# Kernel optimization log

Hardware: AMD Instinct MI355X
Metric: run time of the kernel (lower is better)

## Reference

```python
import jax, jax.numpy as jnp
import numpy as np

BS, N, D_ENT, K, D_IN, D_F, H, L, S = 128, 512, 256, 128, 1024, 256, 128, 2, 64
MAX_ENTITY_NUM = 512.0
TEMP = 1.0
NEG = -1e9


def _ln(x, g, b, eps=1e-5):
    m = jnp.mean(x, -1, keepdims=True)
    v = jnp.mean((x - m) ** 2, -1, keepdims=True)
    return (x - m) * jax.lax.rsqrt(v + eps) * g + b


def setup_inputs() -> dict:
    key = jax.random.key(0)
    ks = jax.random.split(key, 16)
    nrm = lambda k, sh, s=0.02: jax.random.normal(k, sh, jnp.float32) * s
    entity_num = jax.random.randint(ks[0], (BS,), 64, N)
    selected_units = jax.random.randint(ks[1], (BS, S), 0, N + 1) % (entity_num[:, None] + 1)
    selected_units_num = jax.random.randint(ks[2], (BS,), 1, S + 1).at[0].set(S)  # max == S so torch seq_len == S
    return dict(
        embedding=nrm(ks[3], (BS, D_IN), 1.0),
        entity_embedding=nrm(ks[4], (BS, N, D_ENT), 1.0),
        key_w=nrm(ks[5], (K, D_ENT)), key_b=jnp.zeros((K,), jnp.float32),
        q1_w=nrm(ks[6], (D_F, D_IN)), q1_b=jnp.zeros((D_F,), jnp.float32),
        q2_w=nrm(ks[7], (K, D_F)), q2_b=jnp.zeros((K,), jnp.float32),
        e1_w=nrm(ks[8], (D_F, K)), e1_b=jnp.zeros((D_F,), jnp.float32),
        e2_w=nrm(ks[9], (D_IN, D_F)), e2_b=jnp.zeros((D_IN,), jnp.float32),
        end_embedding=nrm(ks[10], (1, K), 0.09),
        lstm_wih=nrm(ks[11], (L, 4 * H, K)),
        lstm_whh=nrm(ks[12], (L, 4 * H, H)),
        ln_ig=jnp.ones((L, 4 * H), jnp.float32), ln_ib=jnp.zeros((L, 4 * H), jnp.float32),
        ln_hg=jnp.ones((L, 4 * H), jnp.float32), ln_hb=jnp.zeros((L, 4 * H), jnp.float32),
        ln_cg=jnp.ones((L, H), jnp.float32), ln_cb=jnp.zeros((L, H), jnp.float32),
        entity_num=entity_num, selected_units=selected_units, selected_units_num=selected_units_num,
    )


def _forward(embedding, entity_embedding, key_w, key_b, q1_w, q1_b, q2_w, q2_b,
             e1_w, e1_b, e2_w, e2_b, end_embedding, lstm_wih, lstm_whh,
             ln_ig, ln_ib, ln_hg, ln_hb, ln_cg, ln_cb,
             entity_num, selected_units, selected_units_num):
    bs = embedding.shape[0]
    ar = jnp.arange(bs)
    # keys: [bs, N+1, K] with end-embedding placed at position entity_num
    key = jnp.einsum('bnd,kd->bnk', entity_embedding, key_w) + key_b
    key = jnp.concatenate([key, jnp.zeros((bs, 1, K), key.dtype)], axis=1)
    key = key.at[ar, entity_num].set(end_embedding[0])
    # entity_reduce_type == 'constant': key_embeddings = embed_mlp(key / MAX_ENTITY_NUM)
    kr = key / MAX_ENTITY_NUM
    key_emb = jax.nn.relu(jnp.einsum('bnk,fk->bnf', kr, e1_w) + e1_b)
    key_emb = jnp.einsum('bnf,df->bnd', key_emb, e2_w) + e2_b  # [bs, N+1, D_IN]
    # precompute per-step masks (cumulative disabling of previously selected units;
    # end token blocked only at step 0, then re-enabled unless selected)
    init_mask = jnp.arange(N + 1)[None, :] < (entity_num + 1)[:, None]
    oh = jax.nn.one_hot(selected_units, N + 1, dtype=jnp.int32)
    prev = jnp.cumsum(oh, axis=1) - oh  # selected strictly before step i
    mask_seq = init_mask[:, None, :] & (prev == 0)  # [bs, S, N+1]
    mask_seq = mask_seq.at[ar, 0, entity_num].set(False)

    def step(carry, xs):
        ae, hs, cs = carry
        i, su_i, m_i = xs
        # query MLP
        x = jax.nn.relu(ae @ q1_w.T + q1_b) @ q2_w.T + q2_b  # [bs, K]
        new_hs, new_cs = [], []
        for l in range(L):  # layer-norm LSTM stack
            gates = _ln(x @ lstm_wih[l].T, ln_ig[l], ln_ib[l]) + _ln(hs[l] @ lstm_whh[l].T, ln_hg[l], ln_hb[l])
            ig, fg, gg, og = jnp.split(gates, 4, axis=-1)
            c = _ln(jax.nn.sigmoid(fg) * cs[l] + jax.nn.sigmoid(ig) * jnp.tanh(gg), ln_cg[l], ln_cb[l])
            h = jax.nn.sigmoid(og) * jnp.tanh(c)
            new_hs.append(h); new_cs.append(c)
            x = h
        logits = jnp.where(m_i, jnp.einsum('bk,bnk->bn', x, key) / TEMP, NEG)
        gate = ((i + 1) <= selected_units_num) & (su_i != entity_num)
        ae = ae + key_emb[ar, su_i] * gate[:, None].astype(ae.dtype)
        return (ae, jnp.stack(new_hs), jnp.stack(new_cs)), logits

    hs0 = jnp.zeros((L, bs, H), embedding.dtype)
    cs0 = jnp.zeros((L, bs, H), embedding.dtype)
    (ae, _, _), logits = jax.lax.scan(
        step, (embedding, hs0, cs0),
        (jnp.arange(S), selected_units.T, jnp.swapaxes(mask_seq, 0, 1)))
    return jnp.swapaxes(logits, 0, 1), ae  # logits [bs, S, N+1]


def reference(embedding, entity_embedding, key_w, key_b, q1_w, q1_b, q2_w, q2_b,
              e1_w, e1_b, e2_w, e2_b, end_embedding, lstm_wih, lstm_whh,
              ln_ig, ln_ib, ln_hg, ln_hb, ln_cg, ln_cb,
              entity_num, selected_units, selected_units_num):
    logits, ae = _forward(embedding, entity_embedding, key_w, key_b, q1_w, q1_b, q2_w, q2_b,
                          e1_w, e1_b, e2_w, e2_b, end_embedding, lstm_wih, lstm_whh,
                          ln_ig, ln_ib, ln_hg, ln_hb, ln_cg, ln_cb,
                          entity_num, selected_units, selected_units_num)
    # torch forward returns (logits, units=None, embedding, selected_units_num); units omitted here
    return logits, ae, selected_units_num
```

## Files before the change

kernel.cpp:

```cpp
#include <hip/hip_runtime.h>
#include <hip/hip_bf16.h>
#include <math.h>

#define BSZ   128
#define NENT  512
#define NP1   513
#define DENT  256
#define KDIM  128
#define DIN   1024
#define DF    256
#define HDIM  128
#define SSTEP 64
#define G4    512
#define NEGV  (-1e9f)
#define INV_MAX (1.0f/512.0f)

typedef float v2f __attribute__((ext_vector_type(2)));
typedef __attribute__((ext_vector_type(8))) short bf16x8;
typedef __attribute__((ext_vector_type(4))) float f32x4;

__device__ inline float sigf(float x){ return 1.f/(1.f+__expf(-x)); }
__device__ inline float tanh_fast(float x){ float e=__expf(2.f*x); return 1.f - 2.f/(e+1.f); }

__device__ inline float wave_sum_partial(float x){
  x += __int_as_float(__builtin_amdgcn_update_dpp(0, __float_as_int(x), 0x111, 0xf, 0xf, true));
  x += __int_as_float(__builtin_amdgcn_update_dpp(0, __float_as_int(x), 0x112, 0xf, 0xf, true));
  x += __int_as_float(__builtin_amdgcn_update_dpp(0, __float_as_int(x), 0x114, 0xf, 0xf, true));
  x += __int_as_float(__builtin_amdgcn_update_dpp(0, __float_as_int(x), 0x118, 0xf, 0xf, true));
  x += __int_as_float(__builtin_amdgcn_update_dpp(0, __float_as_int(x), 0x142, 0xa, 0xf, true));
  x += __int_as_float(__builtin_amdgcn_update_dpp(0, __float_as_int(x), 0x143, 0xc, 0xf, true));
  return x;
}
__device__ inline float wave_sum(float x){
  return __int_as_float(__builtin_amdgcn_readlane(__float_as_int(wave_sum_partial(x)), 63));
}

__device__ inline unsigned pk8(float4 f){
  int r = 0;
  r = __builtin_amdgcn_cvt_pk_fp8_f32(f.x, f.y, r, false);
  r = __builtin_amdgcn_cvt_pk_fp8_f32(f.z, f.w, r, true);
  return (unsigned)r;
}
__device__ inline float dot4_fp8(unsigned w, float4 h, float acc){
  v2f p = __builtin_amdgcn_cvt_pk_f32_fp8((int)w, false);
  acc = fmaf(p.x, h.x, acc); acc = fmaf(p.y, h.y, acc);
  p = __builtin_amdgcn_cvt_pk_f32_fp8((int)w, true);
  acc = fmaf(p.x, h.z, acc); acc = fmaf(p.y, h.w, acc);
  return acc;
}

__device__ inline float2 block_reduce2(float x, float y, float* red){
  float sx0 = wave_sum_partial(x), sy0 = wave_sum_partial(y);
  int w = threadIdx.x>>6;
  __syncthreads();
  if((threadIdx.x&63)==63){ red[w]=sx0; red[8+w]=sy0; }
  __syncthreads();
  float sx=0.f, sy=0.f;
  #pragma unroll
  for(int q=0;q<8;q++){ sx+=red[q]; sy+=red[8+q]; }
  return make_float2(sx,sy);
}

template<bool BKMAJOR, bool RELU, bool GATHER>
__global__ __launch_bounds__(256)
void mfma_gemm(const float* __restrict__ A, const float* __restrict__ B,
               const float* __restrict__ bias, float* __restrict__ C,
               int M, int N, int K,
               const int* __restrict__ gidx, float scale){
  __shared__ ushort Abf[64][72];
  __shared__ ushort Bbf[64][72];
  const int t = threadIdx.x;
  const int bm = blockIdx.x, bn = blockIdx.y;
  const int w = t>>6, l = t&63;
  const int lm = l&15, lg = l>>4;
  const int r0 = w*16;
  f32x4 acc[4];
  #pragma unroll
  for(int f=0;f<4;f++) acc[f] = (f32x4){0.f,0.f,0.f,0.f};

  for(int k0=0;k0<K;k0+=64){
    #pragma unroll
    for(int i=0;i<4;i++){
      int idx = t + i*256;
      int row = idx>>4, c4 = (idx&15)<<2;
      const float* src;
      if(GATHER){
        int gr = bm*64+row;
        src = &A[((size_t)(gr>>6)*NP1 + gidx[gr])*(size_t)K + k0 + c4];
      } else {
        src = &A[((size_t)bm*64+row)*K + k0 + c4];
      }
      float4 v = *(const float4*)src;
      if(GATHER){ v.x*=scale; v.y*=scale; v.z*=scale; v.w*=scale; }
      ushort4 u;
      u.x = __float_as_uint(v.x)>>16; u.y = __float_as_uint(v.y)>>16;
      u.z = __float_as_uint(v.z)>>16; u.w = __float_as_uint(v.w)>>16;
      *(ushort4*)&Abf[row][c4] = u;
    }
    if(!BKMAJOR){
      #pragma unroll
      for(int i=0;i<4;i++){
        int idx = t + i*256;
        int row = idx>>4, c4 = (idx&15)<<2;
        float4 v = *(const float4*)&B[((size_t)bn*64+row)*K + k0 + c4];
        ushort4 u;
        u.x = __float_as_uint(v.x)>>16; u.y = __float_as_uint(v.y)>>16;
        u.z = __float_as_uint(v.z)>>16; u.w = __float_as_uint(v.w)>>16;
        *(ushort4*)&Bbf[row][c4] = u;
      }
    } else {
      #pragma unroll
      for(int i=0;i<4;i++){
        int idx = t + i*256;
        int kr = idx>>4, n4 = (idx&15)<<2;
        float4 v = *(const float4*)&B[(size_t)(k0+kr)*N + bn*64 + n4];
        Bbf[n4+0][kr] = __float_as_uint(v.x)>>16;
        Bbf[n4+1][kr] = __float_as_uint(v.y)>>16;
        Bbf[n4+2][kr] = __float_as_uint(v.z)>>16;
        Bbf[n4+3][kr] = __float_as_uint(v.w)>>16;
      }
    }
    __syncthreads();
    #pragma unroll
    for(int kk=0;kk<64;kk+=32){
      bf16x8 a = *(const bf16x8*)&Abf[r0+lm][kk + lg*8];
      #pragma unroll
      for(int f=0;f<4;f++){
        bf16x8 b = *(const bf16x8*)&Bbf[f*16+lm][kk + lg*8];
        acc[f] = __builtin_amdgcn_mfma_f32_16x16x32_bf16(a, b, acc[f], 0,0,0);
      }
    }
    __syncthreads();
  }
  #pragma unroll
  for(int f=0;f<4;f++){
    int gcol = bn*64 + f*16 + lm;
    float bb = bias ? bias[gcol] : 0.f;
    #pragma unroll
    for(int r=0;r<4;r++){
      int grow = bm*64 + r0 + lg*4 + r;
      float v = acc[f][r] + bb;
      if(RELU) v = fmaxf(v, 0.f);
      C[(size_t)grow*N + gcol] = v;
    }
  }
}

__global__ __launch_bounds__(256)
void key_gemm_mfma(const float* __restrict__ A, const float* __restrict__ W,
                   const float* __restrict__ bias, float* __restrict__ C){
  __shared__ ushort Abf[64][264];
  __shared__ ushort Bbf[128][264];
  __shared__ float bs[128];
  const int t = threadIdx.x;
  const int bm = blockIdx.x;
  #pragma unroll
  for(int i=0;i<16;i++){
    int idx = t + i*256;
    int row = idx>>6, c4 = (idx&63)<<2;
    float4 v = *(const float4*)&A[((size_t)bm*64+row)*256 + c4];
    ushort4 u;
    u.x = __float_as_uint(v.x)>>16; u.y = __float_as_uint(v.y)>>16;
    u.z = __float_as_uint(v.z)>>16; u.w = __float_as_uint(v.w)>>16;
    *(ushort4*)&Abf[row][c4] = u;
  }
  #pragma unroll
  for(int i=0;i<32;i++){
    int idx = t + i*256;
    int row = idx>>6, c4 = (idx&63)<<2;
    float4 v = *(const float4*)&W[(size_t)row*256 + c4];
    ushort4 u;
    u.x = __float_as_uint(v.x)>>16; u.y = __float_as_uint(v.y)>>16;
    u.z = __float_as_uint(v.z)>>16; u.w = __float_as_uint(v.w)>>16;
    *(ushort4*)&Bbf[row][c4] = u;
  }
  if(t<128) bs[t] = bias[t];
  __syncthreads();
  const int w = t>>6, l = t&63;
  const int lm = l&15, lg = l>>4;
  const int r0 = w*16;
  f32x4 acc[8];
  #pragma unroll
  for(int f=0;f<8;f++) acc[f] = (f32x4){0.f,0.f,0.f,0.f};
  #pragma unroll
  for(int k0=0;k0<256;k0+=32){
    bf16x8 a = *(const bf16x8*)&Abf[r0+lm][k0 + lg*8];
    #pragma unroll
    for(int f=0;f<8;f++){
      bf16x8 b = *(const bf16x8*)&Bbf[f*16+lm][k0 + lg*8];
      acc[f] = __builtin_amdgcn_mfma_f32_16x16x32_bf16(a, b, acc[f], 0,0,0);
    }
  }
  #pragma unroll
  for(int f=0;f<8;f++){
    int gcol = f*16 + lm;
    float bb = bs[gcol];
    #pragma unroll
    for(int r=0;r<4;r++){
      int grow = bm*64 + r0 + lg*4 + r;
      size_t orow = (size_t)(grow>>9)*NP1 + (grow&511);
      C[orow*KDIM + gcol] = acc[f][r] + bb;
    }
  }
}

__global__ void fixup_end(const int* __restrict__ en, const float* __restrict__ end_emb,
                          float* __restrict__ key){
  int b = blockIdx.x, k = threadIdx.x;
  int e = en[b];
  key[((size_t)b*NP1 + NENT)*KDIM + k] = 0.f;
  key[((size_t)b*NP1 + e)*KDIM + k] = end_emb[k];
}

__global__ __launch_bounds__(256)
void c0_kernel(const float* __restrict__ q1_w, const float* __restrict__ e2_b,
               float* __restrict__ c0v){
  __shared__ float red[4];
  int f = blockIdx.x, t = threadIdx.x;
  float4 a = *(const float4*)&q1_w[(size_t)f*DIN + t*4];
  float4 e = *(const float4*)&e2_b[t*4];
  float p = a.x*e.x + a.y*e.y + a.z*e.z + a.w*e.w;
  float s = wave_sum_partial(p);
  if((t&63)==63) red[t>>6] = s;
  __syncthreads();
  if(t==0) c0v[f] = red[0]+red[1]+red[2]+red[3];
}

__global__ void prefix_kernel(const float* __restrict__ U0, const float* __restrict__ Q1K,
                              const float* __restrict__ c0v, const float* __restrict__ T1,
                              const int* __restrict__ su, const int* __restrict__ en,
                              const int* __restrict__ sun,
                              float* __restrict__ RU, float* __restrict__ s1,
                              float* __restrict__ ngout){
  int b = blockIdx.x, f = threadIdx.x;
  float acc = U0[b*DF+f];
  float c0f = c0v[f];
  float s1a = 0.f, ng = 0.f;
  int enb = en[b], sunb = sun[b];
  for(int j=0;j<SSTEP;j++){
    int r = b*SSTEP+j;
    float q = Q1K[(size_t)r*DF+f];
    float tt = T1[(size_t)r*DF+f];
    RU[(size_t)r*DF+f] = fmaxf(acc,0.f);
    int sj = su[r];
    float g = ((j+1)<=sunb && sj!=enb) ? 1.f : 0.f;
    acc = fmaf(g, q + c0f, acc);
    s1a = fmaf(g, tt, s1a);
    ng += g;
  }
  s1[b*DF+f]=s1a;
  if(f==0) ngout[b]=ng;
}

__global__ __launch_bounds__(512)
void ln512(float* __restrict__ G, const float* __restrict__ gam, const float* __restrict__ bet){
  __shared__ float red[16];
  size_t r = blockIdx.x;
  int j = threadIdx.x;
  float v = G[r*G4+j];
  float2 s = block_reduce2(v, v*v, red);
  float mu = s.x*(1.f/512.f);
  float rs = rsqrtf(s.y*(1.f/512.f) - mu*mu + 1e-5f);
  G[r*G4+j] = (v-mu)*rs*gam[j] + bet[j];
}

__global__ __launch_bounds__(512)
__attribute__((amdgpu_waves_per_eu(2,2)))
void lstm_serial(const float* __restrict__ wih, const float* __restrict__ whh,
                 const float* __restrict__ G0,
                 const float* __restrict__ ln_ig, const float* __restrict__ ln_ib,
                 const float* __restrict__ ln_hg, const float* __restrict__ ln_hb,
                 const float* __restrict__ ln_cg, const float* __restrict__ ln_cb,
                 float* __restrict__ H1){
  const int b = blockIdx.x;
  const int j = threadIdx.x;
  __shared__ uint4 W0s8[8][512];
  __shared__ uint4 W1s8[8][512];
  __shared__ float h0s[128], h1s[128];
  __shared__ float pvv[512], pv1[512];
  __shared__ float lnA[512], lnB[512], lnC[512], lnD[512], lnE[512], lnF[512];
  __shared__ float red[32];

  #pragma unroll
  for(int c=0;c<8;c++){
    const float* s0 = &whh[(size_t)j*KDIM + c*16];
    uint4 p;
    p.x = pk8(*(const float4*)(s0+ 0));
    p.y = pk8(*(const float4*)(s0+ 4));
    p.z = pk8(*(const float4*)(s0+ 8));
    p.w = pk8(*(const float4*)(s0+12));
    W0s8[c][j] = p;
    const float* s1 = &wih[65536 + (size_t)j*KDIM + c*16];
    uint4 q;
    q.x = pk8(*(const float4*)(s1+ 0));
    q.y = pk8(*(const float4*)(s1+ 4));
    q.z = pk8(*(const float4*)(s1+ 8));
    q.w = pk8(*(const float4*)(s1+12));
    W1s8[c][j] = q;
  }
  uint4 w2p[8];
  #pragma unroll
  for(int c=0;c<8;c++){
    const float* s2 = &whh[65536 + (size_t)j*KDIM + c*16];
    w2p[c].x = pk8(*(const float4*)(s2+ 0));
    w2p[c].y = pk8(*(const float4*)(s2+ 4));
    w2p[c].z = pk8(*(const float4*)(s2+ 8));
    w2p[c].w = pk8(*(const float4*)(s2+12));
  }
  lnA[j] = ln_hg[j];     lnB[j] = ln_hb[j];
  lnC[j] = ln_ig[512+j]; lnD[j] = ln_ib[512+j];
  lnE[j] = ln_hg[512+j]; lnF[j] = ln_hb[512+j];

  float cg0A=0.f,cb0A=0.f,cg0B=0.f,cb0B=0.f;
  float cg1A=0.f,cb1A=0.f,cg1B=0.f,cb1B=0.f;
  float c0rA=0.f,c0rB=0.f,c1rA=0.f,c1rB=0.f;
  if(j<64){
    cg0A=ln_cg[j];      cb0A=ln_cb[j];
    cg0B=ln_cg[j+64];   cb0B=ln_cb[j+64];
    cg1A=ln_cg[128+j];    cb1A=ln_cb[128+j];
    cg1B=ln_cg[128+j+64]; cb1B=ln_cb[128+j+64];
  }
  if(j<128){ h0s[j]=0.f; h1s[j]=0.f; }
  __syncthreads();

  const float4* h04 = (const float4*)h0s;
  const float4* h14 = (const float4*)h1s;
  const int w = j>>6;

  for(int i=0;i<SSTEP;i++){
    float g0a[4], g0b[4];
    if(j<64){
      const float* gp = &G0[((size_t)b*SSTEP+i)*G4];
      #pragma unroll
      for(int k=0;k<4;k++){ g0a[k]=gp[j+128*k]; g0b[k]=gp[j+64+128*k]; }
    }

    float v = 0.f, vb = 0.f;
    #pragma unroll
    for(int c=0;c<8;c++){
      uint4 ww = W0s8[c][j];
      v  = dot4_fp8(ww.x, h04[4*c+0], v );
      vb = dot4_fp8(ww.y, h04[4*c+1], vb);
      v  = dot4_fp8(ww.z, h04[4*c+2], v );
      vb = dot4_fp8(ww.w, h04[4*c+3], vb);
    }
    v += vb;
    float v1 = 0.f, v1b = 0.f;
    #pragma unroll
    for(int c=0;c<8;c++){
      uint4 ww = w2p[c];
      v1  = dot4_fp8(ww.x, h14[4*c+0], v1 );
      v1b = dot4_fp8(ww.y, h14[4*c+1], v1b);
      v1  = dot4_fp8(ww.z, h14[4*c+2], v1 );
      v1b = dot4_fp8(ww.w, h14[4*c+3], v1b);
    }
    v1 += v1b;
    {
      float a  = wave_sum_partial(v);
      float bq = wave_sum_partial(v*v);
      float c2 = wave_sum_partial(v1);
      float d  = wave_sum_partial(v1*v1);
      if((j&63)==63){ red[w]=a; red[8+w]=bq; red[16+w]=c2; red[24+w]=d; }
    }
    pvv[j]=v; pv1[j]=v1;
    __syncthreads();

    if(j<64){
      float S=0.f,S2=0.f;
      #pragma unroll
      for(int q=0;q<8;q++){ S+=red[q]; S2+=red[8+q]; }
      float mu = S*(1.f/512.f);
      float rs = rsqrtf(S2*(1.f/512.f) - mu*mu + 1e-5f);
      float ashA[4], ashB[4];
      #pragma unroll
      for(int k=0;k<4;k++){
        int ia = j + 128*k, ib = j + 64 + 128*k;
        ashA[k] = g0a[k] + (pvv[ia]-mu)*rs*lnA[ia] + lnB[ia];
        ashB[k] = g0b[k] + (pvv[ib]-mu)*rs*lnA[ib] + lnB[ib];
      }
      float cpA = sigf(ashA[1])*c0rA + sigf(ashA[0])*tanh_fast(ashA[2]);
      float cpB = sigf(ashB[1])*c0rB + sigf(ashB[0])*tanh_fast(ashB[2]);
      float s  = wave_sum(cpA+cpB);
      float s2 = wave_sum(cpA*cpA+cpB*cpB);
      float muc = s*(1.f/128.f);
      float rsc = rsqrtf(s2*(1.f/128.f) - muc*muc + 1e-5f);
      c0rA = (cpA-muc)*rsc*cg0A + cb0A;
      c0rB = (cpB-muc)*rsc*cg0B + cb0B;
      h0s[j]    = sigf(ashA[3])*tanh_fast(c0rA);
      h0s[j+64] = sigf(ashB[3])*tanh_fast(c0rB);
    }
    __syncthreads();

    float u = 0.f, ub = 0.f;
    #pragma unroll
    for(int c=0;c<8;c++){
      uint4 ww = W1s8[c][j];
      u  = dot4_fp8(ww.x, h04[4*c+0], u );
      ub = dot4_fp8(ww.y, h04[4*c+1], ub);
      u  = dot4_fp8(ww.z, h04[4*c+2], u );
      ub = dot4_fp8(ww.w, h04[4*c+3], ub);
    }
    u += ub;
    {
      float a  = wave_sum_partial(u);
      float bq = wave_sum_partial(u*u);
      if((j&63)==63){ red[w]=a; red[8+w]=bq; }
    }
    pvv[j]=u;
    __syncthreads();

    if(j<64){
      float Su=0.f,Su2=0.f,Sv=0.f,Sv2=0.f;
      #pragma unroll
      for(int q=0;q<8;q++){ Su+=red[q]; Su2+=red[8+q]; Sv+=red[16+q]; Sv2+=red[24+q]; }
      float muu = Su*(1.f/512.f);
      float rsu = rsqrtf(Su2*(1.f/512.f) - muu*muu + 1e-5f);
      float muv = Sv*(1.f/512.f);
      float rsv = rsqrtf(Sv2*(1.f/512.f) - muv*muv + 1e-5f);
      float ashA[4], ashB[4];
      #pragma unroll
      for(int k=0;k<4;k++){
        int ia = j + 128*k, ib = j + 64 + 128*k;
        ashA[k] = (pvv[ia]-muu)*rsu*lnC[ia] + lnD[ia]
                + (pv1[ia]-muv)*rsv*lnE[ia] + lnF[ia];
        ashB[k] = (pvv[ib]-muu)*rsu*lnC[ib] + lnD[ib]
                + (pv1[ib]-muv)*rsv*lnE[ib] + lnF[ib];
      }
      float cpA = sigf(ashA[1])*c1rA + sigf(ashA[0])*tanh_fast(ashA[2]);
      float cpB = sigf(ashB[1])*c1rB + sigf(ashB[0])*tanh_fast(ashB[2]);
      float s  = wave_sum(cpA+cpB);
      float s2 = wave_sum(cpA*cpA+cpB*cpB);
      float muc = s*(1.f/128.f);
      float rsc = rsqrtf(s2*(1.f/128.f) - muc*muc + 1e-5f);
      c1rA = (cpA-muc)*rsc*cg1A + cb1A;
      c1rB = (cpB-muc)*rsc*cg1B + cb1B;
      float hA = sigf(ashA[3])*tanh_fast(c1rA);
      float hB = sigf(ashB[3])*tanh_fast(c1rB);
      h1s[j]    = hA;
      h1s[j+64] = hB;
      H1[((size_t)b*SSTEP+i)*HDIM + j]      = hA;
      H1[((size_t)b*SSTEP+i)*HDIM + j + 64] = hB;
    }
    __syncthreads();
  }
}

__global__ __launch_bounds__(512)
void logits_kernel(const float* __restrict__ key, const float* __restrict__ H1,
                   const int* __restrict__ en, const int* __restrict__ su,
                   float* __restrict__ out){
  const int b = blockIdx.x;
  const int ihalf = blockIdx.y;
  __shared__ float HsT[128][36];
  __shared__ int firstsel[NP1];
  for(int t=threadIdx.x; t<32*HDIM; t+=512){
    int il = t>>7, k = t&127;
    HsT[k][il] = H1[(size_t)b*SSTEP*HDIM + (size_t)(ihalf*32+il)*HDIM + k];
  }
  for(int t=threadIdx.x; t<NP1; t+=512) firstsel[t] = 1<<30;
  __syncthreads();
  if(threadIdx.x < SSTEP) atomicMin(&firstsel[su[b*SSTEP+threadIdx.x]], (int)threadIdx.x);
  __syncthreads();
  const int enb = en[b];
  const int tn = threadIdx.x & 255;
  const int ig = threadIdx.x >> 8;
  const int i0l = ig*16;
  const int ig0 = ihalf*32 + i0l;
  float acc0[16], acc1[16];
  #pragma unroll
  for(int q=0;q<16;q++){ acc0[q]=0.f; acc1[q]=0.f; }
  const float* kr0 = key + ((size_t)b*NP1 + tn)*KDIM;
  const float* kr1 = key + ((size_t)b*NP1 + tn + 256)*KDIM;
  for(int k=0;k<KDIM;k+=4){
    float4 kv0 = *(const float4*)&kr0[k];
    float4 kv1 = *(const float4*)&kr1[k];
    float k0a[4] = {kv0.x,kv0.y,kv0.z,kv0.w};
    float k1a[4] = {kv1.x,kv1.y,kv1.z,kv1.w};
    #pragma unroll
    for(int kk=0;kk<4;kk++){
      float4 h0 = *(const float4*)&HsT[k+kk][i0l+0];
      float4 h1 = *(const float4*)&HsT[k+kk][i0l+4];
      float4 h2 = *(const float4*)&HsT[k+kk][i0l+8];
      float4 h3 = *(const float4*)&HsT[k+kk][i0l+12];
      float ka = k0a[kk], kb = k1a[kk];
      acc0[ 0]=fmaf(ka,h0.x,acc0[ 0]); acc0[ 1]=fmaf(ka,h0.y,acc0[ 1]);
      acc0[ 2]=fmaf(ka,h0.z,acc0[ 2]); acc0[ 3]=fmaf(ka,h0.w,acc0[ 3]);
      acc0[ 4]=fmaf(ka,h1.x,acc0[ 4]); acc0[ 5]=fmaf(ka,h1.y,acc0[ 5]);
      acc0[ 6]=fmaf(ka,h1.z,acc0[ 6]); acc0[ 7]=fmaf(ka,h1.w,acc0[ 7]);
      acc0[ 8]=fmaf(ka,h2.x,acc0[ 8]); acc0[ 9]=fmaf(ka,h2.y,acc0[ 9]);
      acc0[10]=fmaf(ka,h2.z,acc0[10]); acc0[11]=fmaf(ka,h2.w,acc0[11]);
      acc0[12]=fmaf(ka,h3.x,acc0[12]); acc0[13]=fmaf(ka,h3.y,acc0[13]);
      acc0[14]=fmaf(ka,h3.z,acc0[14]); acc0[15]=fmaf(ka,h3.w,acc0[15]);
      acc1[ 0]=fmaf(kb,h0.x,acc1[ 0]); acc1[ 1]=fmaf(kb,h0.y,acc1[ 1]);
      acc1[ 2]=fmaf(kb,h0.z,acc1[ 2]); acc1[ 3]=fmaf(kb,h0.w,acc1[ 3]);
      acc1[ 4]=fmaf(kb,h1.x,acc1[ 4]); acc1[ 5]=fmaf(kb,h1.y,acc1[ 5]);
      acc1[ 6]=fmaf(kb,h1.z,acc1[ 6]); acc1[ 7]=fmaf(kb,h1.w,acc1[ 7]);
      acc1[ 8]=fmaf(kb,h2.x,acc1[ 8]); acc1[ 9]=fmaf(kb,h2.y,acc1[ 9]);
      acc1[10]=fmaf(kb,h2.z,acc1[10]); acc1[11]=fmaf(kb,h2.w,acc1[11]);
      acc1[12]=fmaf(kb,h3.x,acc1[12]); acc1[13]=fmaf(kb,h3.y,acc1[13]);
      acc1[14]=fmaf(kb,h3.z,acc1[14]); acc1[15]=fmaf(kb,h3.w,acc1[15]);
    }
  }
  const int n0 = tn, n1 = tn + 256;
  const int fs0 = firstsel[n0], fs1 = firstsel[n1];
  #pragma unroll
  for(int q=0;q<16;q++){
    int i = ig0 + q;
    bool m0 = (n0 <= enb) && (fs0 >= i) && !(i==0 && n0==enb);
    bool m1 = (n1 <= enb) && (fs1 >= i) && !(i==0 && n1==enb);
    out[((size_t)b*SSTEP + i)*NP1 + n0] = m0 ? acc0[q] : NEGV;
    out[((size_t)b*SSTEP + i)*NP1 + n1] = m1 ? acc1[q] : NEGV;
  }
  if(threadIdx.x < 32){
    int i = ihalf*32 + threadIdx.x;
    out[((size_t)b*SSTEP + i)*NP1 + 512] = NEGV;
  }
}

__global__ void ae_out_kernel(const float* __restrict__ emb, const float* __restrict__ P,
                              const float* __restrict__ e2_b, const float* __restrict__ ng,
                              const int* __restrict__ sun, float* __restrict__ out){
  const size_t AE_OFF = (size_t)BSZ*SSTEP*NP1;
  const size_t SUN_OFF = AE_OFF + (size_t)BSZ*DIN;
  int idx = blockIdx.x*256+threadIdx.x;
  int b = idx>>10, d = idx&1023;
  out[AE_OFF + idx] = emb[idx] + P[idx] + ng[b]*e2_b[d];
  if(idx < BSZ) out[SUN_OFF + idx] = (float)sun[idx];
}

extern "C" void kernel_launch(void* const* d_in, const int* in_sizes, int n_in,
                              void* d_out, int out_size, void* d_ws, size_t ws_size,
                              hipStream_t stream){
  const float* emb     = (const float*)d_in[0];
  const float* ent     = (const float*)d_in[1];
  const float* key_w   = (const float*)d_in[2];
  const float* key_b   = (const float*)d_in[3];
  const float* q1_w    = (const float*)d_in[4];
  const float* q1_b    = (const float*)d_in[5];
  const float* q2_w    = (const float*)d_in[6];
  const float* q2_b    = (const float*)d_in[7];
  const float* e1_w    = (const float*)d_in[8];
  const float* e1_b    = (const float*)d_in[9];
  const float* e2_w    = (const float*)d_in[10];
  const float* e2_b    = (const float*)d_in[11];
  const float* end_emb = (const float*)d_in[12];
  const float* wih     = (const float*)d_in[13];
  const float* whh     = (const float*)d_in[14];
  const float* ln_ig   = (const float*)d_in[15];
  const float* ln_ib   = (const float*)d_in[16];
  const float* ln_hg   = (const float*)d_in[17];
  const float* ln_hb   = (const float*)d_in[18];
  const float* ln_cg   = (const float*)d_in[19];
  const float* ln_cb   = (const float*)d_in[20];
  const int* en  = (const int*)d_in[21];
  const int* su  = (const int*)d_in[22];
  const int* sun = (const int*)d_in[23];
  float* out = (float*)d_out;
  float* ws  = (float*)d_ws;

  const size_t o_key = 0;
  const size_t o_T1  = o_key + 8404992;
  const size_t o_q1e = o_T1  + 2097152;
  const size_t o_c0  = o_q1e + 65536;
  const size_t o_U0  = o_c0  + 1024;
  const size_t o_Q1K = o_U0  + 32768;
  const size_t o_RU  = o_Q1K + 2097152;
  const size_t o_X   = o_RU  + 2097152;
  const size_t o_G0  = o_X   + 1048576;
  const size_t o_s1  = o_G0  + 4194304;
  const size_t o_ng  = o_s1  + 32768;
  const size_t o_H1  = o_ng  + 1024;
  const size_t o_P   = o_H1  + 1048576;

  key_gemm_mfma<<<1024,256,0,stream>>>(ent, key_w, key_b, ws+o_key);
  fixup_end<<<128,128,0,stream>>>(en, end_emb, ws+o_key);
  mfma_gemm<false,true,true><<<dim3(128,4),256,0,stream>>>(ws+o_key, e1_w, e1_b, ws+o_T1,
                                                           8192,256,128, su, INV_MAX);
  mfma_gemm<true,false,false><<<dim3(4,4),256,0,stream>>>(q1_w, e2_w, nullptr, ws+o_q1e,
                                                          256,256,1024, nullptr, 1.f);
  c0_kernel<<<256,256,0,stream>>>(q1_w, e2_b, ws+o_c0);
  mfma_gemm<false,false,false><<<dim3(2,4),256,0,stream>>>(emb, q1_w, q1_b, ws+o_U0,
                                                           128,256,1024, nullptr, 1.f);
  mfma_gemm<false,false,false><<<dim3(128,4),256,0,stream>>>(ws+o_T1, ws+o_q1e, nullptr, ws+o_Q1K,
                                                             8192,256,256, nullptr, 1.f);
  prefix_kernel<<<128,256,0,stream>>>(ws+o_U0, ws+o_Q1K, ws+o_c0, ws+o_T1, su, en, sun,
                                      ws+o_RU, ws+o_s1, ws+o_ng);
  mfma_gemm<false,false,false><<<dim3(128,2),256,0,stream>>>(ws+o_RU, q2_w, q2_b, ws+o_X,
                                                             8192,128,256, nullptr, 1.f);
  mfma_gemm<false,false,false><<<dim3(128,8),256,0,stream>>>(ws+o_X, wih, nullptr, ws+o_G0,
                                                             8192,512,128, nullptr, 1.f);
  ln512<<<8192,512,0,stream>>>(ws+o_G0, ln_ig, ln_ib);
  lstm_serial<<<128,512,0,stream>>>(wih, whh, ws+o_G0,
                                    ln_ig, ln_ib, ln_hg, ln_hb, ln_cg, ln_cb, ws+o_H1);
  logits_kernel<<<dim3(128,2),512,0,stream>>>(ws+o_key, ws+o_H1, en, su, out);
  mfma_gemm<false,false,false><<<dim3(2,16),256,0,stream>>>(ws+o_s1, e2_w, nullptr, ws+o_P,
                                                            128,1024,256, nullptr, 1.f);
  ae_out_kernel<<<512,256,0,stream>>>(emb, ws+o_P, e2_b, ws+o_ng, sun, out);
}
```

Before: 538.6 us.

## Fuse kernels: end-key fixup, c0 dot, gate GEMM+LayerNorm, AE epilogue; redundant LSTM cell compute

Several small launches are folded into neighbours. The end-embedding fixup moves into the key GEMM epilogue, and the c0 dot product moves into the prefix kernel. The X·Wih GEMM is fused with its 512-wide LayerNorm, and the AE output add is fused into the e2 GEMM. In the LSTM, every wave now computes the cell update redundantly into its own private h copy, which removes one block barrier per layer step. This trades fewer launches and barriers for redundant ALU work and uncached global reads of weights inside the fused GEMM.

```diff
diff --git a/kernel.cpp b/kernel.cpp
--- a/kernel.cpp
+++ b/kernel.cpp
@@ -22,11 +22,15 @@
 __device__ inline float sigf(float x){ return 1.f/(1.f+__expf(-x)); }
 __device__ inline float tanh_fast(float x){ float e=__expf(2.f*x); return 1.f - 2.f/(e+1.f); }
 
-__device__ inline float wave_sum_partial(float x){
+__device__ inline float sum16_partial(float x){
   x += __int_as_float(__builtin_amdgcn_update_dpp(0, __float_as_int(x), 0x111, 0xf, 0xf, true));
   x += __int_as_float(__builtin_amdgcn_update_dpp(0, __float_as_int(x), 0x112, 0xf, 0xf, true));
   x += __int_as_float(__builtin_amdgcn_update_dpp(0, __float_as_int(x), 0x114, 0xf, 0xf, true));
   x += __int_as_float(__builtin_amdgcn_update_dpp(0, __float_as_int(x), 0x118, 0xf, 0xf, true));
+  return x;
+}
+__device__ inline float wave_sum_partial(float x){
+  x = sum16_partial(x);
   x += __int_as_float(__builtin_amdgcn_update_dpp(0, __float_as_int(x), 0x142, 0xa, 0xf, true));
   x += __int_as_float(__builtin_amdgcn_update_dpp(0, __float_as_int(x), 0x143, 0xc, 0xf, true));
   return x;
@@ -148,7 +152,8 @@
 
 __global__ __launch_bounds__(256)
 void key_gemm_mfma(const float* __restrict__ A, const float* __restrict__ W,
-                   const float* __restrict__ bias, float* __restrict__ C){
+                   const float* __restrict__ bias, const int* __restrict__ en,
+                   const float* __restrict__ end_emb, float* __restrict__ C){
   __shared__ ushort Abf[64][264];
   __shared__ ushort Bbf[128][264];
   __shared__ float bs[128];
@@ -195,46 +200,111 @@
   for(int f=0;f<8;f++){
     int gcol = f*16 + lm;
     float bb = bs[gcol];
+    float ev = end_emb[gcol];
     #pragma unroll
     for(int r=0;r<4;r++){
       int grow = bm*64 + r0 + lg*4 + r;
-      size_t orow = (size_t)(grow>>9)*NP1 + (grow&511);
-      C[orow*KDIM + gcol] = acc[f][r] + bb;
-    }
-  }
-}
-
-__global__ void fixup_end(const int* __restrict__ en, const float* __restrict__ end_emb,
-                          float* __restrict__ key){
-  int b = blockIdx.x, k = threadIdx.x;
-  int e = en[b];
-  key[((size_t)b*NP1 + NENT)*KDIM + k] = 0.f;
-  key[((size_t)b*NP1 + e)*KDIM + k] = end_emb[k];
+      int bq = grow>>9, n = grow&511;
+      size_t orow = (size_t)bq*NP1 + n;
+      float v = acc[f][r] + bb;
+      if(n == en[bq]) v = ev;
+      C[orow*KDIM + gcol] = v;
+    }
+  }
 }
 
 __global__ __launch_bounds__(256)
-void c0_kernel(const float* __restrict__ q1_w, const float* __restrict__ e2_b,
-               float* __restrict__ c0v){
-  __shared__ float red[4];
-  int f = blockIdx.x, t = threadIdx.x;
-  float4 a = *(const float4*)&q1_w[(size_t)f*DIN + t*4];
-  float4 e = *(const float4*)&e2_b[t*4];
-  float p = a.x*e.x + a.y*e.y + a.z*e.z + a.w*e.w;
-  float s = wave_sum_partial(p);
-  if((t&63)==63) red[t>>6] = s;
+void g0_gemm_ln(const float* __restrict__ X, const float* __restrict__ W,
+                const float* __restrict__ gam, const float* __restrict__ bet,
+                float* __restrict__ G0){
+  __shared__ ushort Abf[16][136];
+  __shared__ float redS[16][4], redQ[16][4];
+  const int t = threadIdx.x, bm = blockIdx.x;
+  const int w = t>>6, l = t&63, lm = l&15, lg = l>>4;
+  {
+    int idx = t*8;
+    int row = idx>>7, c = idx&127;
+    const float* src = &X[((size_t)bm*16+row)*128 + c];
+    float4 a = *(const float4*)src;
+    float4 d = *(const float4*)(src+4);
+    ushort4 u0, u1;
+    u0.x=__float_as_uint(a.x)>>16; u0.y=__float_as_uint(a.y)>>16;
+    u0.z=__float_as_uint(a.z)>>16; u0.w=__float_as_uint(a.w)>>16;
+    u1.x=__float_as_uint(d.x)>>16; u1.y=__float_as_uint(d.y)>>16;
+    u1.z=__float_as_uint(d.z)>>16; u1.w=__float_as_uint(d.w)>>16;
+    *(ushort4*)&Abf[row][c] = u0;
+    *(ushort4*)&Abf[row][c+4] = u1;
+  }
   __syncthreads();
-  if(t==0) c0v[f] = red[0]+red[1]+red[2]+red[3];
-}
-
-__global__ void prefix_kernel(const float* __restrict__ U0, const float* __restrict__ Q1K,
-                              const float* __restrict__ c0v, const float* __restrict__ T1,
-                              const int* __restrict__ su, const int* __restrict__ en,
-                              const int* __restrict__ sun,
-                              float* __restrict__ RU, float* __restrict__ s1,
-                              float* __restrict__ ngout){
+  f32x4 acc[8];
+  #pragma unroll
+  for(int f=0;f<8;f++) acc[f] = (f32x4){0.f,0.f,0.f,0.f};
+  #pragma unroll
+  for(int kt=0;kt<4;kt++){
+    int k0 = kt*32;
+    bf16x8 a = *(const bf16x8*)&Abf[lm][k0 + lg*8];
+    #pragma unroll
+    for(int f=0;f<8;f++){
+      int brow = w*128 + f*16 + lm;
+      const float* bp = &W[(size_t)brow*128 + k0 + lg*8];
+      float4 b0 = *(const float4*)bp;
+      float4 b1 = *(const float4*)(bp+4);
+      bf16x8 bfr;
+      bfr[0]=(short)(__float_as_uint(b0.x)>>16); bfr[1]=(short)(__float_as_uint(b0.y)>>16);
+      bfr[2]=(short)(__float_as_uint(b0.z)>>16); bfr[3]=(short)(__float_as_uint(b0.w)>>16);
+      bfr[4]=(short)(__float_as_uint(b1.x)>>16); bfr[5]=(short)(__float_as_uint(b1.y)>>16);
+      bfr[6]=(short)(__float_as_uint(b1.z)>>16); bfr[7]=(short)(__float_as_uint(b1.w)>>16);
+      acc[f] = __builtin_amdgcn_mfma_f32_16x16x32_bf16(a, bfr, acc[f], 0,0,0);
+    }
+  }
+  float mu[4], rs[4];
+  #pragma unroll
+  for(int r=0;r<4;r++){
+    float s=0.f, q=0.f;
+    #pragma unroll
+    for(int f=0;f<8;f++){ float x=acc[f][r]; s+=x; q+=x*x; }
+    s = sum16_partial(s);
+    q = sum16_partial(q);
+    if(lm==15){ redS[lg*4+r][w]=s; redQ[lg*4+r][w]=q; }
+  }
+  __syncthreads();
+  #pragma unroll
+  for(int r=0;r<4;r++){
+    int row = lg*4+r;
+    float S = redS[row][0]+redS[row][1]+redS[row][2]+redS[row][3];
+    float Q = redQ[row][0]+redQ[row][1]+redQ[row][2]+redQ[row][3];
+    mu[r] = S*(1.f/512.f);
+    rs[r] = rsqrtf(Q*(1.f/512.f) - mu[r]*mu[r] + 1e-5f);
+  }
+  #pragma unroll
+  for(int f=0;f<8;f++){
+    int col = w*128 + f*16 + lm;
+    float g = gam[col], bt = bet[col];
+    #pragma unroll
+    for(int r=0;r<4;r++){
+      int grow = bm*16 + lg*4 + r;
+      G0[(size_t)grow*G4 + col] = (acc[f][r]-mu[r])*rs[r]*g + bt;
+    }
+  }
+}
+
+__global__ __launch_bounds__(256)
+void prefix_kernel(const float* __restrict__ U0, const float* __restrict__ Q1K,
+                   const float* __restrict__ q1_w, const float* __restrict__ e2_b,
+                   const float* __restrict__ T1,
+                   const int* __restrict__ su, const int* __restrict__ en,
+                   const int* __restrict__ sun,
+                   float* __restrict__ RU, float* __restrict__ s1,
+                   float* __restrict__ ngout){
   int b = blockIdx.x, f = threadIdx.x;
+  float c0f = 0.f;
+  for(int d=0; d<DIN; d+=4){
+    float4 a = *(const float4*)&q1_w[(size_t)f*DIN+d];
+    float4 e = *(const float4*)&e2_b[d];
+    c0f = fmaf(a.x,e.x,c0f); c0f = fmaf(a.y,e.y,c0f);
+    c0f = fmaf(a.z,e.z,c0f); c0f = fmaf(a.w,e.w,c0f);
+  }
   float acc = U0[b*DF+f];
-  float c0f = c0v[f];
   float s1a = 0.f, ng = 0.f;
   int enb = en[b], sunb = sun[b];
   for(int j=0;j<SSTEP;j++){
@@ -253,18 +323,6 @@
 }
 
 __global__ __launch_bounds__(512)
-void ln512(float* __restrict__ G, const float* __restrict__ gam, const float* __restrict__ bet){
-  __shared__ float red[16];
-  size_t r = blockIdx.x;
-  int j = threadIdx.x;
-  float v = G[r*G4+j];
-  float2 s = block_reduce2(v, v*v, red);
-  float mu = s.x*(1.f/512.f);
-  float rs = rsqrtf(s.y*(1.f/512.f) - mu*mu + 1e-5f);
-  G[r*G4+j] = (v-mu)*rs*gam[j] + bet[j];
-}
-
-__global__ __launch_bounds__(512)
 __attribute__((amdgpu_waves_per_eu(2,2)))
 void lstm_serial(const float* __restrict__ wih, const float* __restrict__ whh,
                  const float* __restrict__ G0,
@@ -274,12 +332,13 @@
                  float* __restrict__ H1){
   const int b = blockIdx.x;
   const int j = threadIdx.x;
+  const int w = j>>6, l = j&63;
   __shared__ uint4 W0s8[8][512];
   __shared__ uint4 W1s8[8][512];
-  __shared__ float h0s[128], h1s[128];
-  __shared__ float pvv[512], pv1[512];
+  __shared__ float h0own[8][128], h1own[8][128];
+  __shared__ float pvv[512], pv1[512], pu[512];
   __shared__ float lnA[512], lnB[512], lnC[512], lnD[512], lnE[512], lnF[512];
-  __shared__ float red[32];
+  __shared__ float red[48];
 
   #pragma unroll
   for(int c=0;c<8;c++){
@@ -311,28 +370,24 @@
   lnC[j] = ln_ig[512+j]; lnD[j] = ln_ib[512+j];
   lnE[j] = ln_hg[512+j]; lnF[j] = ln_hb[512+j];
 
-  float cg0A=0.f,cb0A=0.f,cg0B=0.f,cb0B=0.f;
-  float cg1A=0.f,cb1A=0.f,cg1B=0.f,cb1B=0.f;
+  float cg0A=ln_cg[l],     cb0A=ln_cb[l];
+  float cg0B=ln_cg[l+64],  cb0B=ln_cb[l+64];
+  float cg1A=ln_cg[128+l],    cb1A=ln_cb[128+l];
+  float cg1B=ln_cg[128+l+64], cb1B=ln_cb[128+l+64];
   float c0rA=0.f,c0rB=0.f,c1rA=0.f,c1rB=0.f;
-  if(j<64){
-    cg0A=ln_cg[j];      cb0A=ln_cb[j];
-    cg0B=ln_cg[j+64];   cb0B=ln_cb[j+64];
-    cg1A=ln_cg[128+j];    cb1A=ln_cb[128+j];
-    cg1B=ln_cg[128+j+64]; cb1B=ln_cb[128+j+64];
-  }
-  if(j<128){ h0s[j]=0.f; h1s[j]=0.f; }
+  h0own[w][l]=0.f; h0own[w][l+64]=0.f;
+  h1own[w][l]=0.f; h1own[w][l+64]=0.f;
   __syncthreads();
 
-  const float4* h04 = (const float4*)h0s;
-  const float4* h14 = (const float4*)h1s;
-  const int w = j>>6;
+  const float4* h04 = (const float4*)h0own[w];
+  const float4* h14 = (const float4*)h1own[w];
 
   for(int i=0;i<SSTEP;i++){
     float g0a[4], g0b[4];
-    if(j<64){
+    {
       const float* gp = &G0[((size_t)b*SSTEP+i)*G4];
       #pragma unroll
-      for(int k=0;k<4;k++){ g0a[k]=gp[j+128*k]; g0b[k]=gp[j+64+128*k]; }
+      for(int k=0;k<4;k++){ g0a[k]=gp[l+128*k]; g0b[k]=gp[l+64+128*k]; }
     }
 
     float v = 0.f, vb = 0.f;
@@ -360,12 +415,12 @@
       float bq = wave_sum_partial(v*v);
       float c2 = wave_sum_partial(v1);
       float d  = wave_sum_partial(v1*v1);
-      if((j&63)==63){ red[w]=a; red[8+w]=bq; red[16+w]=c2; red[24+w]=d; }
+      if(l==63){ red[w]=a; red[8+w]=bq; red[16+w]=c2; red[24+w]=d; }
     }
     pvv[j]=v; pv1[j]=v1;
     __syncthreads();
 
-    if(j<64){
+    {
       float S=0.f,S2=0.f;
       #pragma unroll
       for(int q=0;q<8;q++){ S+=red[q]; S2+=red[8+q]; }
@@ -374,7 +429,7 @@
       float ashA[4], ashB[4];
       #pragma unroll
       for(int k=0;k<4;k++){
-        int ia = j + 128*k, ib = j + 64 + 128*k;
+        int ia = l + 128*k, ib = l + 64 + 128*k;
         ashA[k] = g0a[k] + (pvv[ia]-mu)*rs*lnA[ia] + lnB[ia];
         ashB[k] = g0b[k] + (pvv[ib]-mu)*rs*lnA[ib] + lnB[ib];
       }
@@ -386,10 +441,9 @@
       float rsc = rsqrtf(s2*(1.f/128.f) - muc*muc + 1e-5f);
       c0rA = (cpA-muc)*rsc*cg0A + cb0A;
       c0rB = (cpB-muc)*rsc*cg0B + cb0B;
-      h0s[j]    = sigf(ashA[3])*tanh_fast(c0rA);
-      h0s[j+64] = sigf(ashB[3])*tanh_fast(c0rB);
-    }
-    __syncthreads();
+      h0own[w][l]    = sigf(ashA[3])*tanh_fast(c0rA);
+      h0own[w][l+64] = sigf(ashB[3])*tanh_fast(c0rB);
+    }
 
     float u = 0.f, ub = 0.f;
     #pragma unroll
@@ -404,15 +458,15 @@
     {
       float a  = wave_sum_partial(u);
       float bq = wave_sum_partial(u*u);
-      if((j&63)==63){ red[w]=a; red[8+w]=bq; }
-    }
-    pvv[j]=u;
+      if(l==63){ red[32+w]=a; red[40+w]=bq; }
+    }
+    pu[j]=u;
     __syncthreads();
 
-    if(j<64){
+    {
       float Su=0.f,Su2=0.f,Sv=0.f,Sv2=0.f;
       #pragma unroll
-      for(int q=0;q<8;q++){ Su+=red[q]; Su2+=red[8+q]; Sv+=red[16+q]; Sv2+=red[24+q]; }
+      for(int q=0;q<8;q++){ Su+=red[32+q]; Su2+=red[40+q]; Sv+=red[16+q]; Sv2+=red[24+q]; }
       float muu = Su*(1.f/512.f);
       float rsu = rsqrtf(Su2*(1.f/512.f) - muu*muu + 1e-5f);
       float muv = Sv*(1.f/512.f);
@@ -420,10 +474,10 @@
       float ashA[4], ashB[4];
       #pragma unroll
       for(int k=0;k<4;k++){
-        int ia = j + 128*k, ib = j + 64 + 128*k;
-        ashA[k] = (pvv[ia]-muu)*rsu*lnC[ia] + lnD[ia]
+        int ia = l + 128*k, ib = l + 64 + 128*k;
+        ashA[k] = (pu[ia]-muu)*rsu*lnC[ia] + lnD[ia]
                 + (pv1[ia]-muv)*rsv*lnE[ia] + lnF[ia];
-        ashB[k] = (pvv[ib]-muu)*rsu*lnC[ib] + lnD[ib]
+        ashB[k] = (pu[ib]-muu)*rsu*lnC[ib] + lnD[ib]
                 + (pv1[ib]-muv)*rsv*lnE[ib] + lnF[ib];
       }
       float cpA = sigf(ashA[1])*c1rA + sigf(ashA[0])*tanh_fast(ashA[2]);
@@ -436,10 +490,12 @@
       c1rB = (cpB-muc)*rsc*cg1B + cb1B;
       float hA = sigf(ashA[3])*tanh_fast(c1rA);
       float hB = sigf(ashB[3])*tanh_fast(c1rB);
-      h1s[j]    = hA;
-      h1s[j+64] = hB;
-      H1[((size_t)b*SSTEP+i)*HDIM + j]      = hA;
-      H1[((size_t)b*SSTEP+i)*HDIM + j + 64] = hB;
+      h1own[w][l]    = hA;
+      h1own[w][l+64] = hB;
+      if(w==0){
+        H1[((size_t)b*SSTEP+i)*HDIM + l]      = hA;
+        H1[((size_t)b*SSTEP+i)*HDIM + l + 64] = hB;
+      }
     }
     __syncthreads();
   }
@@ -517,15 +573,68 @@
   }
 }
 
-__global__ void ae_out_kernel(const float* __restrict__ emb, const float* __restrict__ P,
-                              const float* __restrict__ e2_b, const float* __restrict__ ng,
-                              const int* __restrict__ sun, float* __restrict__ out){
+__global__ __launch_bounds__(256)
+void ae_gemm(const float* __restrict__ A, const float* __restrict__ B,
+             const float* __restrict__ emb, const float* __restrict__ e2_b,
+             const float* __restrict__ ng, const int* __restrict__ sun,
+             float* __restrict__ out){
   const size_t AE_OFF = (size_t)BSZ*SSTEP*NP1;
   const size_t SUN_OFF = AE_OFF + (size_t)BSZ*DIN;
-  int idx = blockIdx.x*256+threadIdx.x;
-  int b = idx>>10, d = idx&1023;
-  out[AE_OFF + idx] = emb[idx] + P[idx] + ng[b]*e2_b[d];
-  if(idx < BSZ) out[SUN_OFF + idx] = (float)sun[idx];
+  __shared__ ushort Abf[64][72];
+  __shared__ ushort Bbf[64][72];
+  const int t = threadIdx.x;
+  const int bm = blockIdx.x, bn = blockIdx.y;
+  const int w = t>>6, l = t&63;
+  const int lm = l&15, lg = l>>4;
+  const int r0 = w*16;
+  f32x4 acc[4];
+  #pragma unroll
+  for(int f=0;f<4;f++) acc[f] = (f32x4){0.f,0.f,0.f,0.f};
+  for(int k0=0;k0<256;k0+=64){
+    #pragma unroll
+    for(int i=0;i<4;i++){
+      int idx = t + i*256;
+      int row = idx>>4, c4 = (idx&15)<<2;
+      float4 v = *(const float4*)&A[((size_t)bm*64+row)*256 + k0 + c4];
+      ushort4 u;
+      u.x = __float_as_uint(v.x)>>16; u.y = __float_as_uint(v.y)>>16;
+      u.z = __float_as_uint(v.z)>>16; u.w = __float_as_uint(v.w)>>16;
+      *(ushort4*)&Abf[row][c4] = u;
+    }
+    #pragma unroll
+    for(int i=0;i<4;i++){
+      int idx = t + i*256;
+      int row = idx>>4, c4 = (idx&15)<<2;
+      float4 v = *(const float4*)&B[((size_t)bn*64+row)*256 + k0 + c4];
+      ushort4 u;
+      u.x = __float_as_uint(v.x)>>16; u.y = __float_as_uint(v.y)>>16;
+      u.z = __float_as_uint(v.z)>>16; u.w = __float_as_uint(v.w)>>16;
+      *(ushort4*)&Bbf[row][c4] = u;
+    }
+    __syncthreads();
+    #pragma unroll
+    for(int kk=0;kk<64;kk+=32){
+      bf16x8 a = *(const bf16x8*)&Abf[r0+lm][kk + lg*8];
+      #pragma unroll
+      for(int f=0;f<4;f++){
+        bf16x8 b = *(const bf16x8*)&Bbf[f*16+lm][kk + lg*8];
+        acc[f] = __builtin_amdgcn_mfma_f32_16x16x32_bf16(a, b, acc[f], 0,0,0);
+      }
+    }
+    __syncthreads();
+  }
+  #pragma unroll
+  for(int f=0;f<4;f++){
+    int gcol = bn*64 + f*16 + lm;
+    float eb = e2_b[gcol];
+    #pragma unroll
+    for(int r=0;r<4;r++){
+      int grow = bm*64 + r0 + lg*4 + r;
+      size_t o = (size_t)grow*DIN + gcol;
+      out[AE_OFF + o] = emb[o] + acc[f][r] + ng[grow]*eb;
+    }
+  }
+  if(bm==0 && bn==0 && t<BSZ) out[SUN_OFF + t] = (float)sun[t];
 }
 
 extern "C" void kernel_launch(void* const* d_in, const int* in_sizes, int n_in,
@@ -561,8 +670,7 @@
   const size_t o_key = 0;
   const size_t o_T1  = o_key + 8404992;
   const size_t o_q1e = o_T1  + 2097152;
-  const size_t o_c0  = o_q1e + 65536;
-  const size_t o_U0  = o_c0  + 1024;
+  const size_t o_U0  = o_q1e + 65536;
   const size_t o_Q1K = o_U0  + 32768;
   const size_t o_RU  = o_Q1K + 2097152;
   const size_t o_X   = o_RU  + 2097152;
@@ -570,30 +678,23 @@
   const size_t o_s1  = o_G0  + 4194304;
   const size_t o_ng  = o_s1  + 32768;
   const size_t o_H1  = o_ng  + 1024;
-  const size_t o_P   = o_H1  + 1048576;
-
-  key_gemm_mfma<<<1024,256,0,stream>>>(ent, key_w, key_b, ws+o_key);
-  fixup_end<<<128,128,0,stream>>>(en, end_emb, ws+o_key);
+
+  key_gemm_mfma<<<1024,256,0,stream>>>(ent, key_w, key_b, en, end_emb, ws+o_key);
   mfma_gemm<false,true,true><<<dim3(128,4),256,0,stream>>>(ws+o_key, e1_w, e1_b, ws+o_T1,
                                                            8192,256,128, su, INV_MAX);
   mfma_gemm<true,false,false><<<dim3(4,4),256,0,stream>>>(q1_w, e2_w, nullptr, ws+o_q1e,
                                                           256,256,1024, nullptr, 1.f);
-  c0_kernel<<<256,256,0,stream>>>(q1_w, e2_b, ws+o_c0);
   mfma_gemm<false,false,false><<<dim3(2,4),256,0,stream>>>(emb, q1_w, q1_b, ws+o_U0,
                                                            128,256,1024, nullptr, 1.f);
   mfma_gemm<false,false,false><<<dim3(128,4),256,0,stream>>>(ws+o_T1, ws+o_q1e, nullptr, ws+o_Q1K,
                                                              8192,256,256, nullptr, 1.f);
-  prefix_kernel<<<128,256,0,stream>>>(ws+o_U0, ws+o_Q1K, ws+o_c0, ws+o_T1, su, en, sun,
+  prefix_kernel<<<128,256,0,stream>>>(ws+o_U0, ws+o_Q1K, q1_w, e2_b, ws+o_T1, su, en, sun,
                                       ws+o_RU, ws+o_s1, ws+o_ng);
   mfma_gemm<false,false,false><<<dim3(128,2),256,0,stream>>>(ws+o_RU, q2_w, q2_b, ws+o_X,
                                                              8192,128,256, nullptr, 1.f);
-  mfma_gemm<false,false,false><<<dim3(128,8),256,0,stream>>>(ws+o_X, wih, nullptr, ws+o_G0,
-                                                             8192,512,128, nullptr, 1.f);
-  ln512<<<8192,512,0,stream>>>(ws+o_G0, ln_ig, ln_ib);
+  g0_gemm_ln<<<512,256,0,stream>>>(ws+o_X, wih, ln_ig, ln_ib, ws+o_G0);
   lstm_serial<<<128,512,0,stream>>>(wih, whh, ws+o_G0,
                                     ln_ig, ln_ib, ln_hg, ln_hb, ln_cg, ln_cb, ws+o_H1);
   logits_kernel<<<dim3(128,2),512,0,stream>>>(ws+o_key, ws+o_H1, en, su, out);
-  mfma_gemm<false,false,false><<<dim3(2,16),256,0,stream>>>(ws+o_s1, e2_w, nullptr, ws+o_P,
-                                                            128,1024,256, nullptr, 1.f);
-  ae_out_kernel<<<512,256,0,stream>>>(emb, ws+o_P, e2_b, ws+o_ng, sun, out);
-}
+  ae_gemm<<<dim3(2,16),256,0,stream>>>(ws+o_s1, e2_w, emb, e2_b, ws+o_ng, sun, out);
+}
```

New measurement: 662.6 us. 23.0% more time.
